# Kernel optimization log

Hardware: AMD Instinct MI355X
Metric: run time of the kernel (lower is better)

The kernel has to match this reference:

```python
import jax, jax.numpy as jnp
import numpy as np

C_TOKEN, C_PAIR, N_HEADS, C_S = 768, 128, 16, 384
C_HID = C_TOKEN // N_HEADS
EPS = 1e-5


def _ln(x):
    # LayerNorm without affine params
    m = jnp.mean(x, axis=-1, keepdims=True)
    v = jnp.mean(jnp.square(x - m), axis=-1, keepdims=True)
    return (x - m) * jax.lax.rsqrt(v + EPS)


def setup_inputs() -> dict:
    key = jax.random.key(0)
    ks = jax.random.split(key, 16)
    B, N = 2, 768
    std = 0.02
    inp = {
        "a": jax.random.normal(ks[0], (B, N, C_TOKEN), jnp.float32),
        "s": jax.random.normal(ks[1], (B, N, C_S), jnp.float32),
        "z": jax.random.normal(ks[2], (B, N, N, C_PAIR), jnp.float32),
        "bias_mask": jax.random.normal(ks[3], (B, N, N), jnp.float32),
        # AdaLN conditioning projections
        "Wg_ada": jax.random.normal(ks[4], (C_S, C_TOKEN), jnp.float32) * std,
        "bg_ada": jnp.zeros((C_TOKEN,), jnp.float32),
        "Wb_ada": jax.random.normal(ks[5], (C_S, C_TOKEN), jnp.float32) * std,
        # QKV
        "Wq": jax.random.normal(ks[6], (C_TOKEN, C_TOKEN), jnp.float32) * std,
        "bq": jnp.zeros((C_TOKEN,), jnp.float32),
        "Wk": jax.random.normal(ks[7], (C_TOKEN, C_TOKEN), jnp.float32) * std,
        "Wv": jax.random.normal(ks[8], (C_TOKEN, C_TOKEN), jnp.float32) * std,
        # pair bias
        "Wpb": jax.random.normal(ks[9], (C_PAIR, N_HEADS), jnp.float32) * std,
        "pn_gamma": jnp.ones((C_PAIR,), jnp.float32),
        "pn_beta": jnp.zeros((C_PAIR,), jnp.float32),
        # gating / output
        "Wgate": jax.random.normal(ks[10], (C_TOKEN, C_TOKEN), jnp.float32) * std,
        "Wout": jax.random.normal(ks[11], (C_TOKEN, C_TOKEN), jnp.float32) * std,
        "Wog": jax.random.normal(ks[12], (C_S, C_TOKEN), jnp.float32) * std,
        "bog": jnp.full((C_TOKEN,), -2.0, jnp.float32),  # adaLN-Zero init
    }
    return inp


def reference(a, s, z, bias_mask, Wg_ada, bg_ada, Wb_ada, Wq, bq, Wk, Wv,
              Wpb, pn_gamma, pn_beta, Wgate, Wout, Wog, bog):
    B, N, _ = a.shape
    # Adaptive LayerNorm: a_ln modulated by conditioning s (AF3 Alg 26)
    a_ln = _ln(a)
    s_ln = _ln(s)
    a_norm = jax.nn.sigmoid(s_ln @ Wg_ada + bg_ada) * a_ln + s_ln @ Wb_ada
    # QKV projections -> [B, H, N, D]
    def split_heads(x):
        return x.reshape(B, N, N_HEADS, C_HID).transpose(0, 2, 1, 3)
    q = split_heads(a_norm @ Wq + bq)
    k = split_heads(a_norm @ Wk)
    v = split_heads(a_norm @ Wv)
    # Pair bias: LayerNorm(z) -> per-head bias [B, H, N, N]
    z_ln = _ln(z) * pn_gamma + pn_beta
    pair_bias = jnp.einsum('bijc,ch->bhij', z_ln, Wpb)
    pair_bias = pair_bias + bias_mask[:, None, :, :]
    # Attention
    logits = jnp.einsum('bhqd,bhkd->bhqk', q, k) / np.float32(np.sqrt(C_HID))
    attn = jax.nn.softmax(logits + pair_bias, axis=-1)
    g = jax.nn.sigmoid(split_heads(a_norm @ Wgate))
    o = g * jnp.einsum('bhqk,bhkd->bhqd', attn, v)  # gated attention output
    o = o.transpose(0, 2, 1, 3).reshape(B, N, C_TOKEN)
    out = o @ Wout
    # Adaptive output gating from raw conditioning s
    out = jax.nn.sigmoid(s @ Wog + bog) * out
    return out
```

## Files before the change

kernel.cpp:

```cpp
#include <hip/hip_runtime.h>
#include <math.h>
#include <stdint.h>

namespace {
constexpr int kN = 768, kCT = 768, kCS = 384, kCP = 128, kNH = 16, kHD = 48;
constexpr float kEps = 1e-5f;
constexpr float kQScale = 0.14433756729740643f;
}

typedef __attribute__((ext_vector_type(8))) short short8;
typedef __attribute__((ext_vector_type(4))) float floatx4;

__device__ __forceinline__ float sigf(float x) { return 1.f / (1.f + expf(-x)); }
__device__ __forceinline__ unsigned short f2bf(float x) {
  uint32_t v = __builtin_bit_cast(uint32_t, x);
  return (unsigned short)((v + 0x7fffu + ((v >> 16) & 1u)) >> 16);
}
__device__ __forceinline__ float bf2f(unsigned short u) {
  uint32_t v = ((uint32_t)u) << 16;
  return __builtin_bit_cast(float, v);
}

#if __has_builtin(__builtin_amdgcn_global_load_lds)
#define HAVE_GLL 1
#define ASYNC_COPY16(gp, lp)                                                     \
  __builtin_amdgcn_global_load_lds((const __attribute__((address_space(1))) void*)(gp), \
                                   (__attribute__((address_space(3))) void*)(lp), 16, 0, 0)
#else
#define HAVE_GLL 0
#endif

__global__ __launch_bounds__(256) void transpose_pack_kernel(
    const float* __restrict__ Wg, const float* __restrict__ Wb,
    const float* __restrict__ Wq, const float* __restrict__ Wk,
    const float* __restrict__ Wv, const float* __restrict__ Wgate,
    const float* __restrict__ Wog, const float* __restrict__ Wout,
    unsigned short* __restrict__ p_adaT, unsigned short* __restrict__ p_qkvT,
    unsigned short* __restrict__ WogT, unsigned short* __restrict__ WoutT) {
  __shared__ float tile[32][33];
  const int cum[8] = {288, 576, 1152, 1728, 2304, 2880, 3168, 3744};
  const int srcK[8] = {384, 384, 768, 768, 768, 768, 384, 768};
  int bid = blockIdx.x;
  int m = 0;
#pragma unroll
  for (int q = 0; q < 8; ++q)
    if (bid >= cum[q]) m = q + 1;
  const int base = m ? cum[m - 1] : 0;
  const int tloc = bid - base;
  const float* src = m == 0 ? Wg : m == 1 ? Wb : m == 2 ? Wq : m == 3 ? Wk
                   : m == 4 ? Wv : m == 5 ? Wgate : m == 6 ? Wog : Wout;
  unsigned short* dst =
      m == 0 ? p_adaT : m == 1 ? (p_adaT + 768 * 384)
    : m == 2 ? p_qkvT : m == 3 ? (p_qkvT + 768 * 768)
    : m == 4 ? (p_qkvT + 2 * 768 * 768) : m == 5 ? (p_qkvT + 3 * 768 * 768)
    : m == 6 ? WogT : WoutT;
  const int K = srcK[m];
  const int bk = tloc / 24, bn = tloc % 24;
  const int k0 = bk * 32, n0 = bn * 32;
  const int tx = threadIdx.x & 31, ty = threadIdx.x >> 5;
#pragma unroll
  for (int r = 0; r < 4; ++r)
    tile[ty + 8 * r][tx] = src[(size_t)(k0 + ty + 8 * r) * 768 + n0 + tx];
  __syncthreads();
#pragma unroll
  for (int r = 0; r < 4; ++r)
    dst[(size_t)(n0 + ty + 8 * r) * K + k0 + tx] = f2bf(tile[tx][ty + 8 * r]);
}

__global__ __launch_bounds__(256) void pack_kernel(
    const float* __restrict__ bg, const float* __restrict__ bq,
    const float* __restrict__ s, const float* __restrict__ Wpb,
    const float* __restrict__ gamma, const float* __restrict__ beta,
    float* __restrict__ pb_ada, float* __restrict__ pb_qk,
    unsigned short* __restrict__ s_bf, unsigned short* __restrict__ gamWT,
    float* __restrict__ pairC) {
  const int T1 = 1536;
  const int T2 = T1 + 3072;
  const int T3 = T2 + 1536 * 384;
  const int T4 = T3 + 2048;
  const int T5 = T4 + 32;
  int idx = blockIdx.x * 256 + threadIdx.x;
  if (idx < T1) {
    pb_ada[idx] = (idx < 768) ? bg[idx] : 0.f;
  } else if (idx < T2) {
    int c = idx - T1;
    pb_qk[c] = (c < 768) ? bq[c] : 0.f;
  } else if (idx < T3) {
    int r = idx - T2;
    s_bf[r] = f2bf(s[r]);
  } else if (idx < T4) {
    int r = idx - T3;
    int h = r >> 7, c = r & 127;
    gamWT[r] = f2bf(gamma[c] * Wpb[c * 16 + h]);
  } else if (idx < T5) {
    int r = idx - T4;
    float acc = 0.f;
    if (r < 16) {
      for (int c = 0; c < 128; ++c) acc += beta[c] * Wpb[c * 16 + r];
      pairC[r] = acc;
    } else {
      int h = r - 16;
      for (int c = 0; c < 128; ++c) acc += gamma[c] * Wpb[c * 16 + h];
      pairC[r] = acc;
    }
  }
}

template <int C>
__global__ __launch_bounds__(256) void ln_kernel(const float* __restrict__ x,
                                                 float* __restrict__ y) {
  constexpr int NV = (C + 255) / 256;
  const int row = blockIdx.x;
  const float* xr = x + (size_t)row * C;
  float vals[NV];
  float s = 0.f, ss = 0.f;
#pragma unroll
  for (int it = 0; it < NV; ++it) {
    int c = threadIdx.x + it * 256;
    float v = (c < C) ? xr[c] : 0.f;
    vals[it] = v;
    s += v;
    ss = fmaf(v, v, ss);
  }
#pragma unroll
  for (int m = 1; m < 64; m <<= 1) { s += __shfl_xor(s, m); ss += __shfl_xor(ss, m); }
  __shared__ float red[8];
  __shared__ float mb[2];
  const int wid = threadIdx.x >> 6, lane = threadIdx.x & 63;
  if (lane == 0) { red[wid * 2] = s; red[wid * 2 + 1] = ss; }
  __syncthreads();
  if (threadIdx.x == 0) {
    float S = red[0] + red[2] + red[4] + red[6];
    float SS = red[1] + red[3] + red[5] + red[7];
    float mean = S / C;
    float var = SS / C - mean * mean;
    mb[0] = mean;
    mb[1] = rsqrtf(var + kEps);
  }
  __syncthreads();
  const float mean = mb[0], rs = mb[1];
#pragma unroll
  for (int it = 0; it < NV; ++it) {
    int c = threadIdx.x + it * 256;
    if (c < C) y[(size_t)row * C + c] = (vals[it] - mean) * rs;
  }
}

template <int C>
__global__ __launch_bounds__(256) void ln_bf_kernel(const float* __restrict__ x,
                                                    unsigned short* __restrict__ y) {
  constexpr int NV = (C + 255) / 256;
  const int row = blockIdx.x;
  const float* xr = x + (size_t)row * C;
  float vals[NV];
  float s = 0.f, ss = 0.f;
#pragma unroll
  for (int it = 0; it < NV; ++it) {
    int c = threadIdx.x + it * 256;
    float v = (c < C) ? xr[c] : 0.f;
    vals[it] = v;
    s += v;
    ss = fmaf(v, v, ss);
  }
#pragma unroll
  for (int m = 1; m < 64; m <<= 1) { s += __shfl_xor(s, m); ss += __shfl_xor(ss, m); }
  __shared__ float red[8];
  __shared__ float mb[2];
  const int wid = threadIdx.x >> 6, lane = threadIdx.x & 63;
  if (lane == 0) { red[wid * 2] = s; red[wid * 2 + 1] = ss; }
  __syncthreads();
  if (threadIdx.x == 0) {
    float S = red[0] + red[2] + red[4] + red[6];
    float SS = red[1] + red[3] + red[5] + red[7];
    float mean = S / C;
    float var = SS / C - mean * mean;
    mb[0] = mean;
    mb[1] = rsqrtf(var + kEps);
  }
  __syncthreads();
  const float mean = mb[0], rs = mb[1];
#pragma unroll
  for (int it = 0; it < NV; ++it) {
    int c = threadIdx.x + it * 256;
    if (c < C) y[(size_t)row * C + c] = f2bf((vals[it] - mean) * rs);
  }
}

__global__ __launch_bounds__(256) void anorm_kernel(const float* __restrict__ gb,
                                                    const float* __restrict__ a_ln,
                                                    unsigned short* __restrict__ a_norm) {
  int idx = blockIdx.x * 256 + threadIdx.x;
  int row = idx / kCT, col = idx % kCT;
  float g = gb[(size_t)row * (2 * kCT) + col];
  float bv = gb[(size_t)row * (2 * kCT) + kCT + col];
  a_norm[idx] = f2bf(sigf(g) * a_ln[idx] + bv);
}

template <int BM>
__global__ __launch_bounds__(256) void gemm_bf_kernel(
    const unsigned short* __restrict__ A, const unsigned short* __restrict__ Wt,
    const float* __restrict__ bias, const float* __restrict__ aux,
    float* __restrict__ C, int M, int Nn, int K, int sig_start) {
  constexpr int TM = BM / 32;
  __shared__ __align__(16) unsigned short As[BM * 32];
  __shared__ __align__(16) unsigned short Bs[128 * 32];
  const int t = threadIdx.x;
  const int wid = t >> 6, lane = t & 63;
  const int quad = lane >> 4, m16 = lane & 15;
  const int wm = (wid >> 1) * (BM / 2), wn = (wid & 1) * 64;
  const int bm = blockIdx.y * BM, bn = blockIdx.x * 128;
  const int swz = quad ^ ((m16 >> 1) & 3);
  const int ci0 = t, ci1 = t + 256;
  const int am0 = ci0 >> 2, ak0 = ((ci0 & 3) ^ ((am0 >> 1) & 3)) * 8;
  const int am1 = ci1 >> 2, ak1 = ((ci1 & 3) ^ ((am1 >> 1) & 3)) * 8;
  const unsigned short* ga0 = A + (size_t)(bm + am0) * K + ak0;
  const unsigned short* ga1 = A + (size_t)(bm + am1) * K + ak1;
  const unsigned short* gw0 = Wt + (size_t)(bn + am0) * K + ak0;
  const unsigned short* gw1 = Wt + (size_t)(bn + am1) * K + ak1;
  floatx4 acc[TM][4] = {};
  for (int k0 = 0; k0 < K; k0 += 32) {
    __syncthreads();
#if HAVE_GLL
    ASYNC_COPY16(ga0 + k0, &As[ci0 * 8]);
    if constexpr (BM == 128) ASYNC_COPY16(ga1 + k0, &As[ci1 * 8]);
    ASYNC_COPY16(gw0 + k0, &Bs[ci0 * 8]);
    ASYNC_COPY16(gw1 + k0, &Bs[ci1 * 8]);
#else
    short8 ra0 = *(const short8*)(ga0 + k0);
    short8 rw0 = *(const short8*)(gw0 + k0);
    short8 rw1 = *(const short8*)(gw1 + k0);
    *(short8*)&As[ci0 * 8] = ra0;
    if constexpr (BM == 128) {
      short8 ra1 = *(const short8*)(ga1 + k0);
      *(short8*)&As[ci1 * 8] = ra1;
    }
    *(short8*)&Bs[ci0 * 8] = rw0;
    *(short8*)&Bs[ci1 * 8] = rw1;
#endif
    __syncthreads();
    short8 af[TM], bfv[4];
#pragma unroll
    for (int tm = 0; tm < TM; ++tm)
      af[tm] = *(const short8*)&As[(wm + tm * 16 + m16) * 32 + swz * 8];
#pragma unroll
    for (int tn = 0; tn < 4; ++tn)
      bfv[tn] = *(const short8*)&Bs[(wn + tn * 16 + m16) * 32 + swz * 8];
#pragma unroll
    for (int tm = 0; tm < TM; ++tm)
#pragma unroll
      for (int tn = 0; tn < 4; ++tn)
        acc[tm][tn] = __builtin_amdgcn_mfma_f32_16x16x32_bf16(af[tm], bfv[tn], acc[tm][tn], 0, 0, 0);
  }
#pragma unroll
  for (int tm = 0; tm < TM; ++tm) {
    const int row0 = bm + wm + tm * 16 + quad * 4;
#pragma unroll
    for (int tn = 0; tn < 4; ++tn) {
      const int col = bn + wn + tn * 16 + m16;
      const float badd = bias ? bias[col] : 0.f;
#pragma unroll
      for (int r = 0; r < 4; ++r) {
        float v = acc[tm][tn][r] + badd;
        if (col >= sig_start) v = sigf(v);
        if (aux) v *= aux[(size_t)(row0 + r) * Nn + col];
        C[(size_t)(row0 + r) * Nn + col] = v;
      }
    }
  }
}

__global__ __launch_bounds__(256, 4) void pairbias3_kernel(
    const float* __restrict__ z, const float* __restrict__ mask,
    const unsigned short* __restrict__ gamWT, const float* __restrict__ pairC,
    unsigned short* __restrict__ pb) {
  __shared__ __align__(16) unsigned short zbf[128 * 136];
  __shared__ float2 pstat[256];
  __shared__ float2 mstat[128];
  const int t = threadIdx.x;
  const int jj = t & 127, half = t >> 7;
  const int b = blockIdx.z, i = blockIdx.y;
  const int j0 = blockIdx.x * 128;
  const float* zrow = &z[((size_t)(b * kN + i) * kN + j0 + jj) * kCP + half * 64];
  float sum = 0.f, ss = 0.f;
#pragma unroll
  for (int g = 0; g < 2; ++g) {
    float4 v[8];
#pragma unroll
    for (int u = 0; u < 8; ++u) v[u] = ((const float4*)zrow)[g * 8 + u];
#pragma unroll
    for (int u = 0; u < 8; ++u) {
      sum += (v[u].x + v[u].y) + (v[u].z + v[u].w);
      ss = fmaf(v[u].x, v[u].x, ss);
      ss = fmaf(v[u].y, v[u].y, ss);
      ss = fmaf(v[u].z, v[u].z, ss);
      ss = fmaf(v[u].w, v[u].w, ss);
    }
#pragma unroll
    for (int k = 0; k < 4; ++k) {
      short8 pk;
      const float4 a = v[2 * k], bb = v[2 * k + 1];
      pk[0] = (short)f2bf(a.x); pk[1] = (short)f2bf(a.y);
      pk[2] = (short)f2bf(a.z); pk[3] = (short)f2bf(a.w);
      pk[4] = (short)f2bf(bb.x); pk[5] = (short)f2bf(bb.y);
      pk[6] = (short)f2bf(bb.z); pk[7] = (short)f2bf(bb.w);
      const int c16 = half * 8 + g * 4 + k;
      *(short8*)&zbf[(jj * 17 + c16) * 8] = pk;
    }
  }
  pstat[t] = make_float2(sum, ss);
  __syncthreads();
  if (t < 128) {
    const float S = pstat[t].x + pstat[t + 128].x;
    const float SS = pstat[t].y + pstat[t + 128].y;
    const float mean = S * (1.f / 128.f);
    const float var = SS * (1.f / 128.f) - mean * mean;
    mstat[t] = make_float2(mean, rsqrtf(var + kEps));
  }
  __syncthreads();
  const int wid = t >> 6, lane = t & 63;
  const int m16 = lane & 15, quad = lane >> 4;
  short8 ga[4];
#pragma unroll
  for (int kk = 0; kk < 4; ++kk)
    ga[kk] = *(const short8*)&gamWT[m16 * 128 + kk * 32 + quad * 8];
  const float4 cb = ((const float4*)pairC)[quad];
  const float4 gs = ((const float4*)pairC)[4 + quad];
#pragma unroll
  for (int u = 0; u < 2; ++u) {
    const int tt = wid * 2 + u;
    const int jloc = tt * 16 + m16;
    floatx4 acc = {};
#pragma unroll
    for (int kk = 0; kk < 4; ++kk) {
      const short8 bf = *(const short8*)&zbf[(jloc * 17 + kk * 4 + quad) * 8];
      acc = __builtin_amdgcn_mfma_f32_16x16x32_bf16(ga[kk], bf, acc, 0, 0, 0);
    }
    const float mean = mstat[jloc].x, rs = mstat[jloc].y;
    const float mk = mask[(size_t)(b * kN + i) * kN + j0 + jloc];
    const size_t obase = ((size_t)(b * kNH + quad * 4) * kN + i) * kN + j0 + jloc;
#pragma unroll
    for (int r = 0; r < 4; ++r) {
      const float gsr = r == 0 ? gs.x : r == 1 ? gs.y : r == 2 ? gs.z : gs.w;
      const float cbr = r == 0 ? cb.x : r == 1 ? cb.y : r == 2 ? cb.z : cb.w;
      const float res = fmaf(rs, fmaf(-mean, gsr, acc[r]), cbr) + mk;
      pb[obase + (size_t)r * kN * kN] = f2bf(res);
    }
  }
}

__global__ __launch_bounds__(1024) void attn_kernel(
    const float* __restrict__ qkvg, const unsigned short* __restrict__ pb,
    unsigned short* __restrict__ o_out) {
  __shared__ float kt[64 * 52];
  __shared__ float vt[64 * 52];
  __shared__ float qs[16][48];
  const int b = blockIdx.z, h = blockIdx.y;
  const int t = threadIdx.x, wid = t >> 6, lane = t & 63;
  const int i = blockIdx.x * 16 + wid;
  const size_t rowi = (size_t)(b * kN + i) * (4 * kCT);
  if (lane < 12) {
    float4 q4 = *(const float4*)&qkvg[rowi + h * kHD + lane * 4];
    qs[wid][lane * 4 + 0] = q4.x * kQScale;
    qs[wid][lane * 4 + 1] = q4.y * kQScale;
    qs[wid][lane * 4 + 2] = q4.z * kQScale;
    qs[wid][lane * 4 + 3] = q4.w * kQScale;
  }
  const int jl = t / 12, d4 = t % 12;
  const bool loader = (t < 768);
  float4 kreg, vreg;
  if (loader) {
    const size_t rowj = (size_t)(b * kN + jl) * (4 * kCT);
    kreg = *(const float4*)&qkvg[rowj + kCT + h * kHD + d4 * 4];
    vreg = *(const float4*)&qkvg[rowj + 2 * kCT + h * kHD + d4 * 4];
  }
  float o[48];
#pragma unroll
  for (int d = 0; d < 48; ++d) o[d] = 0.f;
  float mrun = -INFINITY, lsum = 0.f;
  const unsigned short* pbrow = &pb[((size_t)(b * kNH + h) * kN + i) * kN];
  for (int c = 0; c < 12; ++c) {
    __syncthreads();
    if (loader) {
      *(float4*)&kt[jl * 52 + d4 * 4] = kreg;
      *(float4*)&vt[jl * 52 + d4 * 4] = vreg;
    }
    __syncthreads();
    if (loader && c < 11) {
      const size_t rowj = (size_t)(b * kN + (c + 1) * 64 + jl) * (4 * kCT);
      kreg = *(const float4*)&qkvg[rowj + kCT + h * kHD + d4 * 4];
      vreg = *(const float4*)&qkvg[rowj + 2 * kCT + h * kHD + d4 * 4];
    }
    float l0 = bf2f(pbrow[c * 64 + lane]), l1 = 0.f, l2 = 0.f, l3 = 0.f;
#pragma unroll
    for (int d4i = 0; d4i < 12; ++d4i) {
      float4 kk = *(const float4*)&kt[lane * 52 + d4i * 4];
      float4 qq = *(const float4*)&qs[wid][d4i * 4];
      l0 = fmaf(qq.x, kk.x, l0);
      l1 = fmaf(qq.y, kk.y, l1);
      l2 = fmaf(qq.z, kk.z, l2);
      l3 = fmaf(qq.w, kk.w, l3);
    }
    float logit = (l0 + l1) + (l2 + l3);
    float mx = logit;
#pragma unroll
    for (int m = 1; m < 64; m <<= 1) mx = fmaxf(mx, __shfl_xor(mx, m));
    const float mnew = fmaxf(mrun, mx);
    const float alpha = expf(mrun - mnew);
    const float p = expf(logit - mnew);
    lsum = fmaf(lsum, alpha, p);
#pragma unroll
    for (int d4i = 0; d4i < 12; ++d4i) {
      float4 vv = *(const float4*)&vt[lane * 52 + d4i * 4];
      o[d4i * 4 + 0] = fmaf(o[d4i * 4 + 0], alpha, p * vv.x);
      o[d4i * 4 + 1] = fmaf(o[d4i * 4 + 1], alpha, p * vv.y);
      o[d4i * 4 + 2] = fmaf(o[d4i * 4 + 2], alpha, p * vv.z);
      o[d4i * 4 + 3] = fmaf(o[d4i * 4 + 3], alpha, p * vv.w);
    }
    mrun = mnew;
  }
#pragma unroll
  for (int m = 1; m < 64; m <<= 1) lsum += __shfl_xor(lsum, m);
#pragma unroll
  for (int d = 0; d < 48; ++d) {
#pragma unroll
    for (int m = 1; m < 64; m <<= 1) o[d] += __shfl_xor(o[d], m);
  }
  if (lane == 0) {
    const float inv = 1.f / lsum;
    unsigned short* orow = o_out + (size_t)(b * kN + i) * kCT + h * kHD;
#pragma unroll
    for (int d4i = 0; d4i < 12; ++d4i) {
      float4 g4 = *(const float4*)&qkvg[rowi + 3 * kCT + h * kHD + d4i * 4];
      uint32_t u0 = (uint32_t)f2bf(g4.x * o[d4i * 4 + 0] * inv) |
                    ((uint32_t)f2bf(g4.y * o[d4i * 4 + 1] * inv) << 16);
      uint32_t u1 = (uint32_t)f2bf(g4.z * o[d4i * 4 + 2] * inv) |
                    ((uint32_t)f2bf(g4.w * o[d4i * 4 + 3] * inv) << 16);
      *(uint32_t*)&orow[d4i * 4 + 0] = u0;
      *(uint32_t*)&orow[d4i * 4 + 2] = u1;
    }
  }
}

extern "C" void kernel_launch(void* const* d_in, const int* in_sizes, int n_in,
                              void* d_out, int out_size, void* d_ws, size_t ws_size,
                              hipStream_t stream) {
  const float* a      = (const float*)d_in[0];
  const float* s      = (const float*)d_in[1];
  const float* z      = (const float*)d_in[2];
  const float* mask   = (const float*)d_in[3];
  const float* Wg_ada = (const float*)d_in[4];
  const float* bg_ada = (const float*)d_in[5];
  const float* Wb_ada = (const float*)d_in[6];
  const float* Wq     = (const float*)d_in[7];
  const float* bq     = (const float*)d_in[8];
  const float* Wk     = (const float*)d_in[9];
  const float* Wv     = (const float*)d_in[10];
  const float* Wpb    = (const float*)d_in[11];
  const float* pn_g   = (const float*)d_in[12];
  const float* pn_b   = (const float*)d_in[13];
  const float* Wgate  = (const float*)d_in[14];
  const float* Wout   = (const float*)d_in[15];
  const float* Wog    = (const float*)d_in[16];
  const float* bog    = (const float*)d_in[17];
  float* out = (float*)d_out;

  char* p = (char*)d_ws;
  auto alloc = [&](size_t bytes) -> char* {
    char* r = p;
    p += (bytes + 255) & ~(size_t)255;
    return r;
  };
  float* a_ln  = (float*)alloc((size_t)1536 * 768 * 4);
  float* gb    = (float*)alloc((size_t)1536 * 1536 * 4);
  float* qkvg  = (float*)alloc((size_t)1536 * 3072 * 4);
  float* ogate = (float*)alloc((size_t)1536 * 768 * 4);
  unsigned short* s_ln   = (unsigned short*)alloc((size_t)1536 * 384 * 2);
  unsigned short* a_nrm  = (unsigned short*)alloc((size_t)1536 * 768 * 2);
  unsigned short* s_bf   = (unsigned short*)alloc((size_t)1536 * 384 * 2);
  unsigned short* o_g    = (unsigned short*)alloc((size_t)1536 * 768 * 2);
  unsigned short* pbias  = (unsigned short*)alloc((size_t)2 * 16 * 768 * 768 * 2);
  unsigned short* p_adaT = (unsigned short*)alloc((size_t)1536 * 384 * 2);
  unsigned short* p_qkvT = (unsigned short*)alloc((size_t)3072 * 768 * 2);
  unsigned short* WogT   = (unsigned short*)alloc((size_t)768 * 384 * 2);
  unsigned short* WoutT  = (unsigned short*)alloc((size_t)768 * 768 * 2);
  unsigned short* gamWT  = (unsigned short*)alloc(2048 * 2);
  float* pb_ada = (float*)alloc(1536 * 4);
  float* pb_qk  = (float*)alloc(3072 * 4);
  float* pairC  = (float*)alloc(32 * 4);

  transpose_pack_kernel<<<dim3(3744), 256, 0, stream>>>(
      Wg_ada, Wb_ada, Wq, Wk, Wv, Wgate, Wog, Wout, p_adaT, p_qkvT, WogT, WoutT);
  const int packTot = 1536 + 3072 + 1536 * 384 + 2048 + 32;
  pack_kernel<<<dim3((packTot + 255) / 256), 256, 0, stream>>>(
      bg_ada, bq, s, Wpb, pn_g, pn_b, pb_ada, pb_qk, s_bf, gamWT, pairC);
  ln_kernel<768><<<dim3(1536), 256, 0, stream>>>(a, a_ln);
  ln_bf_kernel<384><<<dim3(1536), 256, 0, stream>>>(s, s_ln);
  gemm_bf_kernel<64><<<dim3(12, 24), 256, 0, stream>>>(
      s_ln, p_adaT, pb_ada, nullptr, gb, 1536, 1536, 384, 1 << 30);
  anorm_kernel<<<dim3(1536 * 768 / 256), 256, 0, stream>>>(gb, a_ln, a_nrm);
  gemm_bf_kernel<128><<<dim3(24, 12), 256, 0, stream>>>(
      a_nrm, p_qkvT, pb_qk, nullptr, qkvg, 1536, 3072, 768, 2304);
  gemm_bf_kernel<64><<<dim3(6, 24), 256, 0, stream>>>(
      s_bf, WogT, bog, nullptr, ogate, 1536, 768, 384, 0);
  pairbias3_kernel<<<dim3(6, 768, 2), 256, 0, stream>>>(z, mask, gamWT, pairC, pbias);
  attn_kernel<<<dim3(48, 16, 2), 1024, 0, stream>>>(qkvg, pbias, o_g);
  gemm_bf_kernel<64><<<dim3(6, 24), 256, 0, stream>>>(
      o_g, WoutT, nullptr, ogate, out, 1536, 768, 768, 1 << 30);
}
```

Measured before the change: 1.211 ms.

## Rewrite attention with bf16 MFMA flash-attention and pre-packed K/V^T buffers

Replaces the scalar fp32 attention kernel, which did one query row per wave with a per-lane dot product and a 48-channel shuffle reduction, with an MFMA-based flash-attention kernel. Each wave handles 16 query rows and computes QK^T and PV with 16x16x32 bf16 MFMA. A new kvpack kernel first converts K to bf16 and V to a transposed bf16 layout. The attention kernel double-buffers those tiles into LDS with async global-to-LDS copies and a swizzle, and shuffles probabilities between lanes with ds_bpermute. This trades fp32 precision in Q, K, V and P for bf16, and adds an extra launch plus a workspace round trip.

Measured after the change: 979.3 us. -19.2%, faster.

```diff
diff --git a/kernel.cpp b/kernel.cpp
--- a/kernel.cpp
+++ b/kernel.cpp
@@ -10,6 +10,7 @@
 
 typedef __attribute__((ext_vector_type(8))) short short8;
 typedef __attribute__((ext_vector_type(4))) float floatx4;
+typedef __attribute__((ext_vector_type(4))) int intx4;
 
 __device__ __forceinline__ float sigf(float x) { return 1.f / (1.f + expf(-x)); }
 __device__ __forceinline__ unsigned short f2bf(float x) {
@@ -19,6 +20,11 @@
 __device__ __forceinline__ float bf2f(unsigned short u) {
   uint32_t v = ((uint32_t)u) << 16;
   return __builtin_bit_cast(float, v);
+}
+__device__ __forceinline__ uint32_t cvtpk(float lo, float hi) {
+  uint32_t r;
+  asm("v_cvt_pk_bf16_f32 %0, %1, %2" : "=v"(r) : "v"(lo), "v"(hi));
+  return r;
 }
 
 #if __has_builtin(__builtin_amdgcn_global_load_lds)
@@ -348,96 +354,199 @@
   }
 }
 
-__global__ __launch_bounds__(1024) void attn_kernel(
-    const float* __restrict__ qkvg, const unsigned short* __restrict__ pb,
+__global__ __launch_bounds__(256) void kvpack_kernel(const float* __restrict__ qkvg,
+                                                     unsigned short* __restrict__ kbf,
+                                                     unsigned short* __restrict__ vtbf) {
+  __shared__ unsigned short vt[48 * 64];
+  const int b = blockIdx.z, h = blockIdx.y, j0 = blockIdx.x * 64;
+  const int bh = b * kNH + h;
+  const int t = threadIdx.x;
+  const int j = t >> 2, dq = t & 3;
+  const size_t rowj = (size_t)(b * kN + j0 + j) * (4 * kCT);
+  {
+    const float* src = &qkvg[rowj + kCT + h * kHD + dq * 12];
+    float4 v0 = ((const float4*)src)[0];
+    float4 v1 = ((const float4*)src)[1];
+    float4 v2 = ((const float4*)src)[2];
+    uint32_t* dst = (uint32_t*)&kbf[((size_t)bh * kN + j0 + j) * kHD + dq * 12];
+    dst[0] = (uint32_t)f2bf(v0.x) | ((uint32_t)f2bf(v0.y) << 16);
+    dst[1] = (uint32_t)f2bf(v0.z) | ((uint32_t)f2bf(v0.w) << 16);
+    dst[2] = (uint32_t)f2bf(v1.x) | ((uint32_t)f2bf(v1.y) << 16);
+    dst[3] = (uint32_t)f2bf(v1.z) | ((uint32_t)f2bf(v1.w) << 16);
+    dst[4] = (uint32_t)f2bf(v2.x) | ((uint32_t)f2bf(v2.y) << 16);
+    dst[5] = (uint32_t)f2bf(v2.z) | ((uint32_t)f2bf(v2.w) << 16);
+  }
+  {
+    const float* src = &qkvg[rowj + 2 * kCT + h * kHD + dq * 12];
+    float4 v0 = ((const float4*)src)[0];
+    float4 v1 = ((const float4*)src)[1];
+    float4 v2 = ((const float4*)src)[2];
+    float vv[12] = {v0.x, v0.y, v0.z, v0.w, v1.x, v1.y, v1.z, v1.w,
+                    v2.x, v2.y, v2.z, v2.w};
+#pragma unroll
+    for (int e = 0; e < 12; ++e) vt[(dq * 12 + e) * 64 + j] = f2bf(vv[e]);
+  }
+  __syncthreads();
+#pragma unroll
+  for (int r = 0; r < 2; ++r) {
+    int ch = t + r * 256;
+    if (ch < 384) {
+      int d = ch >> 3, jo = (ch & 7) * 8;
+      short8 v = *(const short8*)&vt[d * 64 + jo];
+      *(short8*)&vtbf[((size_t)bh * kHD + d) * kN + j0 + jo] = v;
+    }
+  }
+}
+
+__global__ __launch_bounds__(256, 4) void attn2_kernel(
+    const float* __restrict__ qkvg, const unsigned short* __restrict__ kbf,
+    const unsigned short* __restrict__ vtbf, const unsigned short* __restrict__ pb,
     unsigned short* __restrict__ o_out) {
-  __shared__ float kt[64 * 52];
-  __shared__ float vt[64 * 52];
-  __shared__ float qs[16][48];
-  const int b = blockIdx.z, h = blockIdx.y;
+  __shared__ __align__(16) unsigned short lds[4 * 3072];
+  const int b = blockIdx.z, h = blockIdx.y, bh = b * kNH + h;
   const int t = threadIdx.x, wid = t >> 6, lane = t & 63;
-  const int i = blockIdx.x * 16 + wid;
-  const size_t rowi = (size_t)(b * kN + i) * (4 * kCT);
-  if (lane < 12) {
-    float4 q4 = *(const float4*)&qkvg[rowi + h * kHD + lane * 4];
-    qs[wid][lane * 4 + 0] = q4.x * kQScale;
-    qs[wid][lane * 4 + 1] = q4.y * kQScale;
-    qs[wid][lane * 4 + 2] = q4.z * kQScale;
-    qs[wid][lane * 4 + 3] = q4.w * kQScale;
-  }
-  const int jl = t / 12, d4 = t % 12;
-  const bool loader = (t < 768);
-  float4 kreg, vreg;
-  if (loader) {
-    const size_t rowj = (size_t)(b * kN + jl) * (4 * kCT);
-    kreg = *(const float4*)&qkvg[rowj + kCT + h * kHD + d4 * 4];
-    vreg = *(const float4*)&qkvg[rowj + 2 * kCT + h * kHD + d4 * 4];
-  }
-  float o[48];
-#pragma unroll
-  for (int d = 0; d < 48; ++d) o[d] = 0.f;
+  const int m16 = lane & 15, quad = lane >> 4;
+  const int i = blockIdx.x * 64 + wid * 16 + m16;
+  short8 qf[2];
+  {
+    const float* qrow = &qkvg[(size_t)(b * kN + i) * (4 * kCT) + h * kHD];
+    float4 a = *(const float4*)(qrow + quad * 8);
+    float4 bb = *(const float4*)(qrow + quad * 8 + 4);
+    float v0[8] = {a.x, a.y, a.z, a.w, bb.x, bb.y, bb.z, bb.w};
+#pragma unroll
+    for (int e = 0; e < 8; ++e) qf[0][e] = (short)f2bf(v0[e] * kQScale);
+    short8 z8 = {};
+    qf[1] = z8;
+    if (quad < 2) {
+      float4 c = *(const float4*)(qrow + 32 + quad * 8);
+      float4 d = *(const float4*)(qrow + 32 + quad * 8 + 4);
+      float v1[8] = {c.x, c.y, c.z, c.w, d.x, d.y, d.z, d.w};
+#pragma unroll
+      for (int e = 0; e < 8; ++e) qf[1][e] = (short)f2bf(v1[e] * kQScale);
+    }
+  }
+  auto stage = [&](int sel, int c) {
+#pragma unroll
+    for (int l = wid; l < 12; l += 4) {
+      if (l < 6) {
+        const unsigned short* src = kbf + (size_t)bh * (kN * kHD) + c * 3072 + l * 512 + lane * 8;
+#if HAVE_GLL
+        ASYNC_COPY16(src, &lds[sel * 6144 + l * 512 + lane * 8]);
+#else
+        short8 tmp = *(const short8*)src;
+        *(short8*)&lds[sel * 6144 + l * 512 + lane * 8] = tmp;
+#endif
+      } else {
+        const int k = l - 6;
+        const int row = 8 * k + (lane >> 3);
+        const int colsw = ((lane & 7) ^ (lane >> 3)) * 8;
+        const unsigned short* src = vtbf + ((size_t)bh * kHD + row) * kN + c * 64 + colsw;
+#if HAVE_GLL
+        ASYNC_COPY16(src, &lds[sel * 6144 + 3072 + k * 512 + lane * 8]);
+#else
+        short8 tmp = *(const short8*)src;
+        *(short8*)&lds[sel * 6144 + 3072 + k * 512 + lane * 8] = tmp;
+#endif
+      }
+    }
+  };
+  floatx4 oacc[3] = {};
   float mrun = -INFINITY, lsum = 0.f;
-  const unsigned short* pbrow = &pb[((size_t)(b * kNH + h) * kN + i) * kN];
+  const unsigned short* pbrow = &pb[((size_t)bh * kN + i) * kN];
+  const int addrA = (m16 + ((quad & 1) ? 32 : 0)) * 4;
+  const int addrB = addrA + 64;
+  stage(0, 0);
   for (int c = 0; c < 12; ++c) {
     __syncthreads();
-    if (loader) {
-      *(float4*)&kt[jl * 52 + d4 * 4] = kreg;
-      *(float4*)&vt[jl * 52 + d4 * 4] = vreg;
-    }
-    __syncthreads();
-    if (loader && c < 11) {
-      const size_t rowj = (size_t)(b * kN + (c + 1) * 64 + jl) * (4 * kCT);
-      kreg = *(const float4*)&qkvg[rowj + kCT + h * kHD + d4 * 4];
-      vreg = *(const float4*)&qkvg[rowj + 2 * kCT + h * kHD + d4 * 4];
-    }
-    float l0 = bf2f(pbrow[c * 64 + lane]), l1 = 0.f, l2 = 0.f, l3 = 0.f;
-#pragma unroll
-    for (int d4i = 0; d4i < 12; ++d4i) {
-      float4 kk = *(const float4*)&kt[lane * 52 + d4i * 4];
-      float4 qq = *(const float4*)&qs[wid][d4i * 4];
-      l0 = fmaf(qq.x, kk.x, l0);
-      l1 = fmaf(qq.y, kk.y, l1);
-      l2 = fmaf(qq.z, kk.z, l2);
-      l3 = fmaf(qq.w, kk.w, l3);
-    }
-    float logit = (l0 + l1) + (l2 + l3);
-    float mx = logit;
-#pragma unroll
-    for (int m = 1; m < 64; m <<= 1) mx = fmaxf(mx, __shfl_xor(mx, m));
-    const float mnew = fmaxf(mrun, mx);
+    if (c < 11) stage((c + 1) & 1, c + 1);
+    const unsigned short* kb = &lds[(c & 1) * 6144];
+    const unsigned short* vt = kb + 3072;
+    float s[4][4];
+#pragma unroll
+    for (int jt = 0; jt < 4; ++jt) {
+      short8 kf0 = *(const short8*)&kb[(jt * 16 + m16) * 48 + quad * 8];
+      short8 kf1 = *(const short8*)&kb[(jt * 16 + m16) * 48 + 32 + quad * 8];
+      floatx4 acc = {};
+      acc = __builtin_amdgcn_mfma_f32_16x16x32_bf16(kf0, qf[0], acc, 0, 0, 0);
+      acc = __builtin_amdgcn_mfma_f32_16x16x32_bf16(kf1, qf[1], acc, 0, 0, 0);
+      ushort4 pbv = *(const ushort4*)&pbrow[c * 64 + jt * 16 + quad * 4];
+      s[jt][0] = acc[0] + bf2f(pbv.x);
+      s[jt][1] = acc[1] + bf2f(pbv.y);
+      s[jt][2] = acc[2] + bf2f(pbv.z);
+      s[jt][3] = acc[3] + bf2f(pbv.w);
+    }
+    float smax = s[0][0];
+#pragma unroll
+    for (int jt = 0; jt < 4; ++jt)
+#pragma unroll
+      for (int r = 0; r < 4; ++r) smax = fmaxf(smax, s[jt][r]);
+    float cm = fmaxf(smax, __shfl_xor(smax, 16));
+    cm = fmaxf(cm, __shfl_xor(cm, 32));
+    const float mnew = fmaxf(mrun, cm);
     const float alpha = expf(mrun - mnew);
-    const float p = expf(logit - mnew);
-    lsum = fmaf(lsum, alpha, p);
-#pragma unroll
-    for (int d4i = 0; d4i < 12; ++d4i) {
-      float4 vv = *(const float4*)&vt[lane * 52 + d4i * 4];
-      o[d4i * 4 + 0] = fmaf(o[d4i * 4 + 0], alpha, p * vv.x);
-      o[d4i * 4 + 1] = fmaf(o[d4i * 4 + 1], alpha, p * vv.y);
-      o[d4i * 4 + 2] = fmaf(o[d4i * 4 + 2], alpha, p * vv.z);
-      o[d4i * 4 + 3] = fmaf(o[d4i * 4 + 3], alpha, p * vv.w);
-    }
+    float p[4][4];
+    float psum = 0.f;
+#pragma unroll
+    for (int jt = 0; jt < 4; ++jt)
+#pragma unroll
+      for (int r = 0; r < 4; ++r) {
+        p[jt][r] = expf(s[jt][r] - mnew);
+        psum += p[jt][r];
+      }
+    psum += __shfl_xor(psum, 16);
+    psum += __shfl_xor(psum, 32);
+    lsum = fmaf(lsum, alpha, psum);
     mrun = mnew;
-  }
-#pragma unroll
-  for (int m = 1; m < 64; m <<= 1) lsum += __shfl_xor(lsum, m);
-#pragma unroll
-  for (int d = 0; d < 48; ++d) {
-#pragma unroll
-    for (int m = 1; m < 64; m <<= 1) o[d] += __shfl_xor(o[d], m);
-  }
-  if (lane == 0) {
-    const float inv = 1.f / lsum;
-    unsigned short* orow = o_out + (size_t)(b * kN + i) * kCT + h * kHD;
-#pragma unroll
-    for (int d4i = 0; d4i < 12; ++d4i) {
-      float4 g4 = *(const float4*)&qkvg[rowi + 3 * kCT + h * kHD + d4i * 4];
-      uint32_t u0 = (uint32_t)f2bf(g4.x * o[d4i * 4 + 0] * inv) |
-                    ((uint32_t)f2bf(g4.y * o[d4i * 4 + 1] * inv) << 16);
-      uint32_t u1 = (uint32_t)f2bf(g4.z * o[d4i * 4 + 2] * inv) |
-                    ((uint32_t)f2bf(g4.w * o[d4i * 4 + 3] * inv) << 16);
-      *(uint32_t*)&orow[d4i * 4 + 0] = u0;
-      *(uint32_t*)&orow[d4i * 4 + 2] = u1;
-    }
+    uint32_t pk[4][2];
+#pragma unroll
+    for (int jt = 0; jt < 4; ++jt) {
+      pk[jt][0] = cvtpk(p[jt][0], p[jt][1]);
+      pk[jt][1] = cvtpk(p[jt][2], p[jt][3]);
+    }
+#pragma unroll
+    for (int dt = 0; dt < 3; ++dt)
+#pragma unroll
+      for (int r = 0; r < 4; ++r) oacc[dt][r] *= alpha;
+#pragma unroll
+    for (int kp = 0; kp < 2; ++kp) {
+      const int tA = 2 * kp, tB = 2 * kp + 1;
+      uint32_t xA0 = (uint32_t)__builtin_amdgcn_ds_bpermute(addrA, (int)pk[tA][0]);
+      uint32_t xA1 = (uint32_t)__builtin_amdgcn_ds_bpermute(addrA, (int)pk[tA][1]);
+      uint32_t yA0 = (uint32_t)__builtin_amdgcn_ds_bpermute(addrA, (int)pk[tB][0]);
+      uint32_t yA1 = (uint32_t)__builtin_amdgcn_ds_bpermute(addrA, (int)pk[tB][1]);
+      uint32_t xB0 = (uint32_t)__builtin_amdgcn_ds_bpermute(addrB, (int)pk[tA][0]);
+      uint32_t xB1 = (uint32_t)__builtin_amdgcn_ds_bpermute(addrB, (int)pk[tA][1]);
+      uint32_t yB0 = (uint32_t)__builtin_amdgcn_ds_bpermute(addrB, (int)pk[tB][0]);
+      uint32_t yB1 = (uint32_t)__builtin_amdgcn_ds_bpermute(addrB, (int)pk[tB][1]);
+      const bool hi = quad >= 2;
+      intx4 pi;
+      pi[0] = (int)(hi ? yA0 : xA0);
+      pi[1] = (int)(hi ? yA1 : xA1);
+      pi[2] = (int)(hi ? yB0 : xB0);
+      pi[3] = (int)(hi ? yB1 : xB1);
+      const short8 pf = __builtin_bit_cast(short8, pi);
+#pragma unroll
+      for (int dt = 0; dt < 3; ++dt) {
+        const int colsw = ((kp * 4 + quad) ^ (m16 & 7)) * 8;
+        short8 vf = *(const short8*)&vt[(dt * 16 + m16) * 64 + colsw];
+        oacc[dt] = __builtin_amdgcn_mfma_f32_16x16x32_bf16(vf, pf, oacc[dt], 0, 0, 0);
+      }
+    }
+  }
+  const float inv = 1.f / lsum;
+  const float* grow = &qkvg[(size_t)(b * kN + i) * (4 * kCT) + 3 * kCT + h * kHD];
+  unsigned short* orow = &o_out[(size_t)(b * kN + i) * kCT + h * kHD];
+#pragma unroll
+  for (int dt = 0; dt < 3; ++dt) {
+    float4 g4 = *(const float4*)&grow[dt * 16 + quad * 4];
+    const float o0 = oacc[dt][0] * inv * g4.x;
+    const float o1 = oacc[dt][1] * inv * g4.y;
+    const float o2 = oacc[dt][2] * inv * g4.z;
+    const float o3 = oacc[dt][3] * inv * g4.w;
+    uint32_t u0 = (uint32_t)f2bf(o0) | ((uint32_t)f2bf(o1) << 16);
+    uint32_t u1 = (uint32_t)f2bf(o2) | ((uint32_t)f2bf(o3) << 16);
+    *(uint32_t*)&orow[dt * 16 + quad * 4 + 0] = u0;
+    *(uint32_t*)&orow[dt * 16 + quad * 4 + 2] = u1;
   }
 }
 
@@ -483,6 +592,8 @@
   unsigned short* p_qkvT = (unsigned short*)alloc((size_t)3072 * 768 * 2);
   unsigned short* WogT   = (unsigned short*)alloc((size_t)768 * 384 * 2);
   unsigned short* WoutT  = (unsigned short*)alloc((size_t)768 * 768 * 2);
+  unsigned short* kbf    = (unsigned short*)alloc((size_t)32 * 768 * 48 * 2);
+  unsigned short* vtbf   = (unsigned short*)alloc((size_t)32 * 48 * 768 * 2);
   unsigned short* gamWT  = (unsigned short*)alloc(2048 * 2);
   float* pb_ada = (float*)alloc(1536 * 4);
   float* pb_qk  = (float*)alloc(3072 * 4);
@@ -503,7 +614,8 @@
   gemm_bf_kernel<64><<<dim3(6, 24), 256, 0, stream>>>(
       s_bf, WogT, bog, nullptr, ogate, 1536, 768, 384, 0);
   pairbias3_kernel<<<dim3(6, 768, 2), 256, 0, stream>>>(z, mask, gamWT, pairC, pbias);
-  attn_kernel<<<dim3(48, 16, 2), 1024, 0, stream>>>(qkvg, pbias, o_g);
+  kvpack_kernel<<<dim3(12, 16, 2), 256, 0, stream>>>(qkvg, kbf, vtbf);
+  attn2_kernel<<<dim3(12, 16, 2), 256, 0, stream>>>(qkvg, kbf, vtbf, pbias, o_g);
   gemm_bf_kernel<64><<<dim3(6, 24), 256, 0, stream>>>(
       o_g, WoutT, nullptr, ogate, out, 1536, 768, 768, 1 << 30);
 }
```
